# Performance work log

Hardware: AMD Instinct MI355X
Metric: run time of the kernel (lower is better)

## Reference

```python
import jax, jax.numpy as jnp
import numpy as np

B, T, C, SIZE = 2, 4096, 1024, 1024
ROPE_DIM = 64
GAMMA = 0.96


def setup_inputs() -> dict:
    key = jax.random.key(0)
    ks = jax.random.split(key, 8)
    x = jax.random.normal(ks[0], (B, T, C), dtype=jnp.float32)
    group_mask = jax.random.randint(ks[1], (B, T), 0, 2).astype(jnp.float32)
    att_mask = jnp.ones((B, T), dtype=jnp.float32)
    # torch init: randn(in, out) / in
    W_Q = jax.random.normal(ks[2], (C, SIZE), dtype=jnp.float32) / C
    W_K = jax.random.normal(ks[3], (C, SIZE), dtype=jnp.float32) / C
    W_V = jax.random.normal(ks[4], (C, SIZE), dtype=jnp.float32) / C
    fc_w = jax.random.normal(ks[5], (SIZE, SIZE), dtype=jnp.float32) / np.float32(np.sqrt(SIZE))
    fc_b = jnp.zeros((SIZE,), dtype=jnp.float32)
    return dict(x=x, group_mask=group_mask, att_mask=att_mask,
                W_Q=W_Q, W_K=W_K, W_V=W_V, fc_w=fc_w, fc_b=fc_b)


def _rope(t, offset):
    # lucidrains rotate_queries_or_keys: rotate first ROPE_DIM features of
    # the last dim, interleaved-pair rotation, positions along axis -2.
    seq = t.shape[-2]
    inv = 1.0 / (10000.0 ** (jnp.arange(0, ROPE_DIM, 2, dtype=jnp.float32) / ROPE_DIM))
    pos = jnp.arange(seq, dtype=jnp.float32) + offset
    freqs = pos[:, None] * inv[None, :]              # [T, D/2]
    freqs = jnp.repeat(freqs, 2, axis=-1)            # [T, D]
    cos, sin = jnp.cos(freqs), jnp.sin(freqs)
    t_rot, t_pass = t[..., :ROPE_DIM], t[..., ROPE_DIM:]
    x1, x2 = t_rot[..., 0::2], t_rot[..., 1::2]
    rot_half = jnp.stack([-x2, x1], axis=-1).reshape(t_rot.shape)
    t_rot = t_rot * cos + rot_half * sin
    return jnp.concatenate([t_rot, t_pass], axis=-1)


def reference(x, group_mask, att_mask, W_Q, W_K, W_V, fc_w, fc_b):
    Bx, Tx, _ = x.shape
    # _qkv with apply_rope=True, apply_act=True (ReLU)
    Q = jax.nn.relu(_rope(x @ W_Q, 0))               # [B,T,SIZE]
    K = jax.nn.relu(_rope(x @ W_K, 0))
    V = jax.nn.relu(x @ W_V)
    n = jnp.arange(Tx)[:, None]
    m = jnp.arange(Tx)[None, :]
    causal = (n >= m)
    # decay mask D[n,m] = gamma^(n-m) for n>=m else 0
    D = jnp.where(causal, jnp.float32(GAMMA) ** (n - m).astype(jnp.float32), 0.0)
    # group mask G[b,n,m] = group_mask[b, n-m] for n>=m else 0
    idx = jnp.clip(n - m, 0, Tx - 1)                 # [T,T]
    G = group_mask[:, idx] * causal.astype(x.dtype)  # [B,T,T]
    A = jnp.einsum('bnd,bmd->bnm', Q, K)
    A = A * att_mask[:, :, None]                     # attention mask
    A = A * D[None, :, :]                            # decay mask
    A = A * G                                        # group mask
    y = jnp.einsum('bnm,bmd->bnd', A, V)
    y = y @ fc_w + fc_b
    return y
```

## Files before the change

kernel.cpp:

```cpp
#include <hip/hip_runtime.h>
#include <stdint.h>

typedef __attribute__((ext_vector_type(4))) float f32x4;
typedef __attribute__((ext_vector_type(8))) __bf16 bf16x8;
typedef __attribute__((ext_vector_type(4))) unsigned short u16x4;
typedef __attribute__((ext_vector_type(8))) unsigned short u16x8;

#define DEV __device__ __forceinline__

DEV unsigned short f2bf(float f) {
  union { float f; unsigned int u; } v; v.f = f;
  unsigned int r = v.u + 0x7fffu + ((v.u >> 16) & 1u);
  return (unsigned short)(r >> 16);
}

DEV void gl_lds16(const void* g, void* l) {
  __builtin_amdgcn_global_load_lds(
      (const __attribute__((address_space(1))) unsigned int*)g,
      (__attribute__((address_space(3))) unsigned int*)l, 16, 0, 0);
}


__global__ void prep_rope(float* __restrict__ costab, float* __restrict__ sintab) {
  int idx = blockIdx.x * 256 + threadIdx.x;
  int n = idx >> 6, c = idx & 63, j = c >> 1;
  float inv = powf(10000.0f, -(float)(2 * j) / 64.0f);
  float ang = (float)n * inv;
  costab[idx] = cosf(ang);
  sintab[idx] = sinf(ang);
}

__global__ void prep_wtab(const float* __restrict__ gm, float* __restrict__ wtab) {
  int t = threadIdx.x;
  int b = t >> 9, d = t & 511;
  wtab[t] = gm[b * 4096 + d] * powf(0.96f, (float)d);
}

__global__ void cvt_x(const float* __restrict__ x, unsigned short* __restrict__ xb) {
  size_t i8 = ((size_t)blockIdx.x * 256 + threadIdx.x) * 8;
  float4 a = *(const float4*)(x + i8);
  float4 b = *(const float4*)(x + i8 + 4);
  u16x8 o;
  o[0] = f2bf(a.x); o[1] = f2bf(a.y); o[2] = f2bf(a.z); o[3] = f2bf(a.w);
  o[4] = f2bf(b.x); o[5] = f2bf(b.y); o[6] = f2bf(b.z); o[7] = f2bf(b.w);
  *(u16x8*)(xb + i8) = o;
}

__global__ void transpose_cvt(const float* __restrict__ src, unsigned short* __restrict__ dst) {
  __shared__ float tile[32][33];
  int tx = threadIdx.x & 31, ty = threadIdx.x >> 5;
  int c0 = blockIdx.x * 32, r0 = blockIdx.y * 32;
  #pragma unroll
  for (int j = 0; j < 4; j++)
    tile[ty + 8 * j][tx] = src[(size_t)(r0 + ty + 8 * j) * 1024 + c0 + tx];
  __syncthreads();
  #pragma unroll
  for (int j = 0; j < 4; j++)
    dst[(size_t)(c0 + ty + 8 * j) * 1024 + r0 + tx] = f2bf(tile[tx][ty + 8 * j]);
}

template<int EPI>
__global__ void __launch_bounds__(256, 2)
gemm128(const unsigned short* __restrict__ A,
        const unsigned short* __restrict__ Bt,
        unsigned short* __restrict__ q_out,
        unsigned short* __restrict__ k_out,
        unsigned short* __restrict__ vt_out,
        const float* __restrict__ costab,
        const float* __restrict__ sintab,
        float* __restrict__ f_out,
        const float* __restrict__ bias)
{
  constexpr int K = 1024;
  __shared__ char smem[32768];
  char* a_sm = smem;
  char* b_sm = smem + 16384;
  const int tid = threadIdx.x;
  const int lane = tid & 63;
  const int w = tid >> 6;
  const int wm = w >> 1, wn = w & 1;
  const int bm = blockIdx.x, bn = blockIdx.y;

  const f32x4 fz = {0.f, 0.f, 0.f, 0.f};
  f32x4 acc[4][4];
  #pragma unroll
  for (int i = 0; i < 4; i++)
    #pragma unroll
    for (int j = 0; j < 4; j++) acc[i][j] = fz;

  const unsigned short* Abase = A + (size_t)bm * 128 * K;
  const unsigned short* Bbase = Bt + (size_t)bn * 128 * K;

  for (int k0 = 0; k0 < K; k0 += 64) {
    __syncthreads();
    #pragma unroll
    for (int i = 0; i < 4; i++) {
      int tg = i * 256 + tid;
      int row = tg >> 3;
      int sl = (tg & 7) ^ (row & 7);
      gl_lds16(Abase + (size_t)row * K + k0 + sl * 8, a_sm + tg * 16);
    }
    #pragma unroll
    for (int i = 0; i < 4; i++) {
      int tg = i * 256 + tid;
      int row = tg >> 3;
      int sl = (tg & 7) ^ (row & 7);
      gl_lds16(Bbase + (size_t)row * K + k0 + sl * 8, b_sm + tg * 16);
    }
    __syncthreads();
    #pragma unroll
    for (int ks = 0; ks < 2; ks++) {
      int kb = ks * 64 + ((lane >> 4) << 4);
      bf16x8 af[4], bfv[4];
      #pragma unroll
      for (int f = 0; f < 4; f++) {
        int ar = wm * 64 + f * 16 + (lane & 15);
        af[f] = *(const bf16x8*)(a_sm + ar * 128 + (kb ^ ((ar & 7) << 4)));
        int br = wn * 64 + f * 16 + (lane & 15);
        bfv[f] = *(const bf16x8*)(b_sm + br * 128 + (kb ^ ((br & 7) << 4)));
      }
      #pragma unroll
      for (int fm = 0; fm < 4; fm++)
        #pragma unroll
        for (int fn = 0; fn < 4; fn++)
          acc[fm][fn] = __builtin_amdgcn_mfma_f32_16x16x32_bf16(af[fm], bfv[fn], acc[fm][fn], 0, 0, 0);
    }
  }

  const int rbase = bm * 128 + wm * 64 + ((lane >> 4) << 2);
  const int cbase = bn * 128 + wn * 64;

  if constexpr (EPI == 0) {
    #pragma unroll
    for (int fn = 0; fn < 4; fn++) {
      int col = cbase + fn * 16 + (lane & 15);
      int which = col >> 10;
      int c = col & 1023;
      #pragma unroll
      for (int fm = 0; fm < 4; fm++) {
        int row0 = rbase + fm * 16;
        float vals[4];
        #pragma unroll
        for (int r = 0; r < 4; r++) vals[r] = acc[fm][fn][r];
        if (which < 2) {
          if (c < 64) {
            #pragma unroll
            for (int r = 0; r < 4; r++) {
              float p = __shfl_xor(vals[r], 1);
              int n = (row0 + r) & 4095;
              float cs = costab[n * 64 + c];
              float sn = sintab[n * 64 + c];
              float rh = (c & 1) ? p : -p;
              vals[r] = vals[r] * cs + rh * sn;
            }
          }
          unsigned short* dst = (which == 0) ? q_out : k_out;
          #pragma unroll
          for (int r = 0; r < 4; r++) {
            float v = vals[r] > 0.f ? vals[r] : 0.f;
            dst[(size_t)(row0 + r) * 1024 + c] = f2bf(v);
          }
        } else {
          u16x4 sv;
          #pragma unroll
          for (int r = 0; r < 4; r++) {
            float v = vals[r] > 0.f ? vals[r] : 0.f;
            sv[r] = f2bf(v);
          }
          *(u16x4*)(vt_out + (size_t)c * 8192 + row0) = sv;
        }
      }
    }
  } else {
    #pragma unroll
    for (int fn = 0; fn < 4; fn++) {
      int col = cbase + fn * 16 + (lane & 15);
      float bv = bias[col];
      #pragma unroll
      for (int fm = 0; fm < 4; fm++) {
        int row0 = rbase + fm * 16;
        #pragma unroll
        for (int r = 0; r < 4; r++)
          f_out[(size_t)(row0 + r) * 1024 + col] = acc[fm][fn][r] + bv;
      }
    }
  }
}

__global__ void __launch_bounds__(512, 2)
attn_kernel(const unsigned short* __restrict__ Qb,
            const unsigned short* __restrict__ Kb,
            const unsigned short* __restrict__ Vt,
            const float* __restrict__ wtab,
            const float* __restrict__ att_mask,
            unsigned short* __restrict__ Yb)
{
  __shared__ char smem[49152];
  __shared__ float wl[320];
  char* k_sm = smem;
  char* q_sm = smem + 40960;
  char* p_sm = smem;

  const int tid = threadIdx.x;
  const int lane = tid & 63;
  const int w = tid >> 6;
  const int q0 = blockIdx.x * 64;
  const int b = blockIdx.y;
  const int base = b * 4096;
  const int kv0 = q0 - 256;

  if (tid < 320) wl[tid] = wtab[b * 512 + tid];

  const int wq = w >> 2, wk = w & 3;
  const f32x4 fz = {0.f, 0.f, 0.f, 0.f};
  f32x4 sacc[2][5];
  #pragma unroll
  for (int i = 0; i < 2; i++)
    #pragma unroll
    for (int j = 0; j < 5; j++) sacc[i][j] = fz;

  for (int c0 = 0; c0 < 1024; c0 += 64) {
    __syncthreads();
    {
      int row = tid >> 3;
      int sl = (tid & 7) ^ (row & 7);
      gl_lds16(Qb + (size_t)(base + q0 + row) * 1024 + c0 + sl * 8, q_sm + tid * 16);
    }
    #pragma unroll
    for (int i = 0; i < 5; i++) {
      int tg = i * 512 + tid;
      int row = tg >> 3;
      int sl = (tg & 7) ^ (row & 7);
      int m = kv0 + row; m = m < 0 ? 0 : m;
      gl_lds16(Kb + (size_t)(base + m) * 1024 + c0 + sl * 8, k_sm + tg * 16);
    }
    __syncthreads();
    #pragma unroll
    for (int ks = 0; ks < 2; ks++) {
      int kb = ks * 64 + ((lane >> 4) << 4);
      bf16x8 af[2], bfv[5];
      #pragma unroll
      for (int f = 0; f < 2; f++) {
        int ar = wq * 32 + f * 16 + (lane & 15);
        af[f] = *(const bf16x8*)(q_sm + ar * 128 + (kb ^ ((ar & 7) << 4)));
      }
      #pragma unroll
      for (int f = 0; f < 5; f++) {
        int br = wk * 80 + f * 16 + (lane & 15);
        bfv[f] = *(const bf16x8*)(k_sm + br * 128 + (kb ^ ((br & 7) << 4)));
      }
      #pragma unroll
      for (int fm = 0; fm < 2; fm++)
        #pragma unroll
        for (int fj = 0; fj < 5; fj++)
          sacc[fm][fj] = __builtin_amdgcn_mfma_f32_16x16x32_bf16(af[fm], bfv[fj], sacc[fm][fj], 0, 0, 0);
    }
  }
  __syncthreads();

  #pragma unroll
  for (int fm = 0; fm < 2; fm++) {
    #pragma unroll
    for (int fj = 0; fj < 5; fj++) {
      int jj = wk * 80 + fj * 16 + (lane & 15);
      int m = kv0 + jj;
      #pragma unroll
      for (int r = 0; r < 4; r++) {
        int i = wq * 32 + fm * 16 + ((lane >> 4) << 2) + r;
        int d = 256 + i - jj;
        float wgt = (d >= 0 && m >= 0) ? wl[d] : 0.f;
        *(unsigned short*)(p_sm + i * 640 + ((jj * 2) ^ ((i & 7) << 4))) =
            f2bf(sacc[fm][fj][r] * wgt);
      }
    }
  }
  __syncthreads();

  f32x4 yacc[4][8];
  #pragma unroll
  for (int i = 0; i < 4; i++)
    #pragma unroll
    for (int j = 0; j < 8; j++) yacc[i][j] = fz;

  for (int kt = 0; kt < 10; kt++) {
    int kb = kt * 64 + ((lane >> 4) << 4);
    bf16x8 pa[4], vb[8];
    #pragma unroll
    for (int f = 0; f < 4; f++) {
      int i = f * 16 + (lane & 15);
      pa[f] = *(const bf16x8*)(p_sm + i * 640 + (kb ^ ((i & 7) << 4)));
    }
    int kvi = kt * 32 + ((lane >> 4) << 3);
    int m = kv0 + kvi; m = m < 0 ? 0 : m;
    #pragma unroll
    for (int f = 0; f < 8; f++) {
      int col = w * 128 + f * 16 + (lane & 15);
      vb[f] = *(const bf16x8*)(Vt + (size_t)col * 8192 + base + m);
    }
    #pragma unroll
    for (int fm = 0; fm < 4; fm++)
      #pragma unroll
      for (int fn = 0; fn < 8; fn++)
        yacc[fm][fn] = __builtin_amdgcn_mfma_f32_16x16x32_bf16(pa[fm], vb[fn], yacc[fm][fn], 0, 0, 0);
  }

  #pragma unroll
  for (int fm = 0; fm < 4; fm++) {
    #pragma unroll
    for (int r = 0; r < 4; r++) {
      int n = q0 + fm * 16 + ((lane >> 4) << 2) + r;
      float am = att_mask[base + n];
      #pragma unroll
      for (int fn = 0; fn < 8; fn++) {
        int col = w * 128 + fn * 16 + (lane & 15);
        Yb[(size_t)(base + n) * 1024 + col] = f2bf(yacc[fm][fn][r] * am);
      }
    }
  }
}

extern "C" void kernel_launch(void* const* d_in, const int* in_sizes, int n_in,
                              void* d_out, int out_size, void* d_ws, size_t ws_size,
                              hipStream_t stream)
{
  (void)in_sizes; (void)n_in; (void)out_size;
  const float* x   = (const float*)d_in[0];
  const float* gm  = (const float*)d_in[1];
  const float* am  = (const float*)d_in[2];
  const float* wq  = (const float*)d_in[3];
  const float* wk  = (const float*)d_in[4];
  const float* wv  = (const float*)d_in[5];
  const float* fcw = (const float*)d_in[6];
  const float* fcb = (const float*)d_in[7];
  float* out = (float*)d_out;

  char* p = (char*)d_ws;
  unsigned short* xb    = (unsigned short*)p; p += (size_t)8192 * 1024 * 2;
  unsigned short* Qb    = (unsigned short*)p; p += (size_t)8192 * 1024 * 2;
  unsigned short* Kb    = (unsigned short*)p; p += (size_t)8192 * 1024 * 2;
  unsigned short* Vt    = (unsigned short*)p; p += (size_t)8192 * 1024 * 2;
  unsigned short* Ybuf  = (unsigned short*)p; p += (size_t)8192 * 1024 * 2;
  unsigned short* WqkvT = (unsigned short*)p; p += (size_t)3072 * 1024 * 2;
  unsigned short* FcwT  = (unsigned short*)p; p += (size_t)1024 * 1024 * 2;
  float* costab = (float*)p; p += (size_t)4096 * 64 * 4;
  float* sintab = (float*)p; p += (size_t)4096 * 64 * 4;
  float* wtab   = (float*)p; p += 4096;
  if ((size_t)(p - (char*)d_ws) > ws_size) return;

  prep_rope<<<1024, 256, 0, stream>>>(costab, sintab);
  prep_wtab<<<1, 1024, 0, stream>>>(gm, wtab);
  cvt_x<<<4096, 256, 0, stream>>>(x, xb);
  transpose_cvt<<<dim3(32, 32), 256, 0, stream>>>(wq, WqkvT);
  transpose_cvt<<<dim3(32, 32), 256, 0, stream>>>(wk, WqkvT + (size_t)1024 * 1024);
  transpose_cvt<<<dim3(32, 32), 256, 0, stream>>>(wv, WqkvT + (size_t)2048 * 1024);
  transpose_cvt<<<dim3(32, 32), 256, 0, stream>>>(fcw, FcwT);

  gemm128<0><<<dim3(64, 24), 256, 0, stream>>>(xb, WqkvT, Qb, Kb, Vt, costab, sintab, nullptr, nullptr);
  attn_kernel<<<dim3(64, 2), 512, 0, stream>>>(Qb, Kb, Vt, wtab, am, Ybuf);
  gemm128<1><<<dim3(64, 8), 256, 0, stream>>>(Ybuf, FcwT, nullptr, nullptr, nullptr, nullptr, nullptr, out, fcb);
}
```

Before: 244.9 us.

## Merge prep launches, remap GEMM blocks across XCDs, split attention into 32-row tiles

Fuses the rope and decay-table prep kernels into one launch and the four weight transposes into one 3D-grid launch, cutting launch overhead. Both GEMMs now use a 1D grid with an XCD-aware block remap (id&7 chunking) so neighbouring tiles share L2. The attention kernel moves from 64 to 32 query rows per block, doubling the grid to 256 blocks for better CU occupancy. It also drops the LDS staging of Q/K in favour of direct global bf16x8 loads, and adds a fast unclamped V-load path.

```diff
diff --git a/kernel.cpp b/kernel.cpp
--- a/kernel.cpp
+++ b/kernel.cpp
@@ -21,19 +21,19 @@
 }
 
 
-__global__ void prep_rope(float* __restrict__ costab, float* __restrict__ sintab) {
+__global__ void prep_tabs(const float* __restrict__ gm,
+                          float* __restrict__ costab, float* __restrict__ sintab,
+                          float* __restrict__ wtab) {
   int idx = blockIdx.x * 256 + threadIdx.x;
   int n = idx >> 6, c = idx & 63, j = c >> 1;
   float inv = powf(10000.0f, -(float)(2 * j) / 64.0f);
   float ang = (float)n * inv;
   costab[idx] = cosf(ang);
   sintab[idx] = sinf(ang);
-}
-
-__global__ void prep_wtab(const float* __restrict__ gm, float* __restrict__ wtab) {
-  int t = threadIdx.x;
-  int b = t >> 9, d = t & 511;
-  wtab[t] = gm[b * 4096 + d] * powf(0.96f, (float)d);
+  if (idx < 1024) {
+    int b = idx >> 9, d = idx & 511;
+    wtab[idx] = gm[b * 4096 + d] * powf(0.96f, (float)d);
+  }
 }
 
 __global__ void cvt_x(const float* __restrict__ x, unsigned short* __restrict__ xb) {
@@ -46,8 +46,13 @@
   *(u16x8*)(xb + i8) = o;
 }
 
-__global__ void transpose_cvt(const float* __restrict__ src, unsigned short* __restrict__ dst) {
+__global__ void transpose_cvt4(const float* __restrict__ s0, const float* __restrict__ s1,
+                               const float* __restrict__ s2, const float* __restrict__ s3,
+                               unsigned short* __restrict__ d0, unsigned short* __restrict__ d3) {
   __shared__ float tile[32][33];
+  int z = blockIdx.z;
+  const float* src = (z == 0) ? s0 : (z == 1) ? s1 : (z == 2) ? s2 : s3;
+  unsigned short* dst = (z == 3) ? d3 : d0 + (size_t)z * 1024 * 1024;
   int tx = threadIdx.x & 31, ty = threadIdx.x >> 5;
   int c0 = blockIdx.x * 32, r0 = blockIdx.y * 32;
   #pragma unroll
@@ -79,7 +84,12 @@
   const int lane = tid & 63;
   const int w = tid >> 6;
   const int wm = w >> 1, wn = w & 1;
-  const int bm = blockIdx.x, bn = blockIdx.y;
+
+  const int id = blockIdx.x;
+  const int chunk = gridDim.x >> 3;
+  const int nid = (id & 7) * chunk + (id >> 3);
+  const int bm = nid & 63;
+  const int bn = nid >> 6;
 
   const f32x4 fz = {0.f, 0.f, 0.f, 0.f};
   f32x4 acc[4][4];
@@ -195,124 +205,118 @@
             const float* __restrict__ att_mask,
             unsigned short* __restrict__ Yb)
 {
-  __shared__ char smem[49152];
-  __shared__ float wl[320];
-  char* k_sm = smem;
-  char* q_sm = smem + 40960;
-  char* p_sm = smem;
+  __shared__ alignas(16) unsigned char p_sm[32 * 640];
+  __shared__ float wl[512];
 
   const int tid = threadIdx.x;
   const int lane = tid & 63;
   const int w = tid >> 6;
-  const int q0 = blockIdx.x * 64;
-  const int b = blockIdx.y;
+
+  const int id = blockIdx.x + blockIdx.y * 128;
+  const int nid = (id & 7) * 32 + (id >> 3);
+  const int qb = nid & 127;
+  const int b = nid >> 7;
+
+  const int q0 = qb * 32;
   const int base = b * 4096;
   const int kv0 = q0 - 256;
 
-  if (tid < 320) wl[tid] = wtab[b * 512 + tid];
+  if (tid < 512) wl[tid] = wtab[b * 512 + tid];
 
   const int wq = w >> 2, wk = w & 3;
+  const int l15 = lane & 15, lhi = lane >> 4;
+
+  const unsigned short* qptr =
+      Qb + (size_t)(base + q0 + wq * 16 + l15) * 1024 + lhi * 8;
+  const unsigned short* krow[5];
+  #pragma unroll
+  for (int f = 0; f < 5; f++) {
+    int m = kv0 + wk * 80 + f * 16 + l15;
+    m = m < 0 ? 0 : (m > 4095 ? 4095 : m);
+    krow[f] = Kb + (size_t)(base + m) * 1024 + lhi * 8;
+  }
+
   const f32x4 fz = {0.f, 0.f, 0.f, 0.f};
-  f32x4 sacc[2][5];
+  f32x4 sacc[5];
+  #pragma unroll
+  for (int f = 0; f < 5; f++) sacc[f] = fz;
+
+  for (int kk = 0; kk < 32; ++kk) {
+    bf16x8 af = *(const bf16x8*)(qptr + kk * 32);
+    #pragma unroll
+    for (int f = 0; f < 5; f++) {
+      bf16x8 bfv = *(const bf16x8*)(krow[f] + kk * 32);
+      sacc[f] = __builtin_amdgcn_mfma_f32_16x16x32_bf16(af, bfv, sacc[f], 0, 0, 0);
+    }
+  }
+
+  __syncthreads();
+
+  #pragma unroll
+  for (int f = 0; f < 5; f++) {
+    int jj = wk * 80 + f * 16 + l15;
+    int m = kv0 + jj;
+    #pragma unroll
+    for (int r = 0; r < 4; r++) {
+      int i = wq * 16 + lhi * 4 + r;
+      int d = 256 + i - jj;
+      float wgt = (d >= 0 && m >= 0) ? wl[d] : 0.f;
+      *(unsigned short*)(p_sm + i * 640 + ((jj * 2) ^ ((i & 7) << 4))) =
+          f2bf(sacc[f][r] * wgt);
+    }
+  }
+  __syncthreads();
+
+  f32x4 yacc[2][8];
   #pragma unroll
   for (int i = 0; i < 2; i++)
     #pragma unroll
-    for (int j = 0; j < 5; j++) sacc[i][j] = fz;
-
-  for (int c0 = 0; c0 < 1024; c0 += 64) {
-    __syncthreads();
-    {
-      int row = tid >> 3;
-      int sl = (tid & 7) ^ (row & 7);
-      gl_lds16(Qb + (size_t)(base + q0 + row) * 1024 + c0 + sl * 8, q_sm + tid * 16);
-    }
-    #pragma unroll
-    for (int i = 0; i < 5; i++) {
-      int tg = i * 512 + tid;
-      int row = tg >> 3;
-      int sl = (tg & 7) ^ (row & 7);
-      int m = kv0 + row; m = m < 0 ? 0 : m;
-      gl_lds16(Kb + (size_t)(base + m) * 1024 + c0 + sl * 8, k_sm + tg * 16);
-    }
-    __syncthreads();
-    #pragma unroll
-    for (int ks = 0; ks < 2; ks++) {
-      int kb = ks * 64 + ((lane >> 4) << 4);
-      bf16x8 af[2], bfv[5];
-      #pragma unroll
-      for (int f = 0; f < 2; f++) {
-        int ar = wq * 32 + f * 16 + (lane & 15);
-        af[f] = *(const bf16x8*)(q_sm + ar * 128 + (kb ^ ((ar & 7) << 4)));
-      }
-      #pragma unroll
-      for (int f = 0; f < 5; f++) {
-        int br = wk * 80 + f * 16 + (lane & 15);
-        bfv[f] = *(const bf16x8*)(k_sm + br * 128 + (kb ^ ((br & 7) << 4)));
-      }
-      #pragma unroll
-      for (int fm = 0; fm < 2; fm++)
-        #pragma unroll
-        for (int fj = 0; fj < 5; fj++)
-          sacc[fm][fj] = __builtin_amdgcn_mfma_f32_16x16x32_bf16(af[fm], bfv[fj], sacc[fm][fj], 0, 0, 0);
-    }
-  }
-  __syncthreads();
-
-  #pragma unroll
-  for (int fm = 0; fm < 2; fm++) {
-    #pragma unroll
-    for (int fj = 0; fj < 5; fj++) {
-      int jj = wk * 80 + fj * 16 + (lane & 15);
-      int m = kv0 + jj;
-      #pragma unroll
-      for (int r = 0; r < 4; r++) {
-        int i = wq * 32 + fm * 16 + ((lane >> 4) << 2) + r;
-        int d = 256 + i - jj;
-        float wgt = (d >= 0 && m >= 0) ? wl[d] : 0.f;
-        *(unsigned short*)(p_sm + i * 640 + ((jj * 2) ^ ((i & 7) << 4))) =
-            f2bf(sacc[fm][fj][r] * wgt);
-      }
-    }
-  }
-  __syncthreads();
-
-  f32x4 yacc[4][8];
-  #pragma unroll
-  for (int i = 0; i < 4; i++)
-    #pragma unroll
     for (int j = 0; j < 8; j++) yacc[i][j] = fz;
 
-  for (int kt = 0; kt < 10; kt++) {
-    int kb = kt * 64 + ((lane >> 4) << 4);
-    bf16x8 pa[4], vb[8];
-    #pragma unroll
-    for (int f = 0; f < 4; f++) {
-      int i = f * 16 + (lane & 15);
-      pa[f] = *(const bf16x8*)(p_sm + i * 640 + (kb ^ ((i & 7) << 4)));
-    }
-    int kvi = kt * 32 + ((lane >> 4) << 3);
-    int m = kv0 + kvi; m = m < 0 ? 0 : m;
-    #pragma unroll
-    for (int f = 0; f < 8; f++) {
-      int col = w * 128 + f * 16 + (lane & 15);
-      vb[f] = *(const bf16x8*)(Vt + (size_t)col * 8192 + base + m);
-    }
-    #pragma unroll
-    for (int fm = 0; fm < 4; fm++)
+  const bool fastv = (kv0 >= 0) && (kv0 <= 3776);
+  const unsigned short* vptr[8];
+  #pragma unroll
+  for (int f = 0; f < 8; f++) {
+    int col = w * 128 + f * 16 + l15;
+    vptr[f] = Vt + (size_t)col * 8192 + base + kv0 + lhi * 8;
+  }
+
+  for (int kt = 0; kt < 10; ++kt) {
+    bf16x8 pa[2], vb[8];
+    #pragma unroll
+    for (int fm = 0; fm < 2; fm++) {
+      int row = fm * 16 + l15;
+      int cp = kt * 64 + lhi * 16;
+      pa[fm] = *(const bf16x8*)(p_sm + row * 640 + (cp ^ ((row & 7) << 4)));
+    }
+    if (fastv) {
+      #pragma unroll
+      for (int f = 0; f < 8; f++) vb[f] = *(const bf16x8*)(vptr[f] + kt * 32);
+    } else {
+      int m = kv0 + kt * 32 + lhi * 8;
+      m = m < 0 ? 0 : (m > 4088 ? 4088 : m);
+      #pragma unroll
+      for (int f = 0; f < 8; f++) {
+        int col = w * 128 + f * 16 + l15;
+        vb[f] = *(const bf16x8*)(Vt + (size_t)col * 8192 + base + m);
+      }
+    }
+    #pragma unroll
+    for (int fm = 0; fm < 2; fm++)
       #pragma unroll
       for (int fn = 0; fn < 8; fn++)
         yacc[fm][fn] = __builtin_amdgcn_mfma_f32_16x16x32_bf16(pa[fm], vb[fn], yacc[fm][fn], 0, 0, 0);
   }
 
   #pragma unroll
-  for (int fm = 0; fm < 4; fm++) {
+  for (int fm = 0; fm < 2; fm++) {
     #pragma unroll
     for (int r = 0; r < 4; r++) {
-      int n = q0 + fm * 16 + ((lane >> 4) << 2) + r;
+      int n = q0 + fm * 16 + lhi * 4 + r;
       float am = att_mask[base + n];
       #pragma unroll
       for (int fn = 0; fn < 8; fn++) {
-        int col = w * 128 + fn * 16 + (lane & 15);
+        int col = w * 128 + fn * 16 + l15;
         Yb[(size_t)(base + n) * 1024 + col] = f2bf(yacc[fm][fn][r] * am);
       }
     }
@@ -347,15 +351,11 @@
   float* wtab   = (float*)p; p += 4096;
   if ((size_t)(p - (char*)d_ws) > ws_size) return;
 
-  prep_rope<<<1024, 256, 0, stream>>>(costab, sintab);
-  prep_wtab<<<1, 1024, 0, stream>>>(gm, wtab);
+  prep_tabs<<<1024, 256, 0, stream>>>(gm, costab, sintab, wtab);
   cvt_x<<<4096, 256, 0, stream>>>(x, xb);
-  transpose_cvt<<<dim3(32, 32), 256, 0, stream>>>(wq, WqkvT);
-  transpose_cvt<<<dim3(32, 32), 256, 0, stream>>>(wk, WqkvT + (size_t)1024 * 1024);
-  transpose_cvt<<<dim3(32, 32), 256, 0, stream>>>(wv, WqkvT + (size_t)2048 * 1024);
-  transpose_cvt<<<dim3(32, 32), 256, 0, stream>>>(fcw, FcwT);
-
-  gemm128<0><<<dim3(64, 24), 256, 0, stream>>>(xb, WqkvT, Qb, Kb, Vt, costab, sintab, nullptr, nullptr);
-  attn_kernel<<<dim3(64, 2), 512, 0, stream>>>(Qb, Kb, Vt, wtab, am, Ybuf);
-  gemm128<1><<<dim3(64, 8), 256, 0, stream>>>(Ybuf, FcwT, nullptr, nullptr, nullptr, nullptr, nullptr, out, fcb);
-}
+  transpose_cvt4<<<dim3(32, 32, 4), 256, 0, stream>>>(wq, wk, wv, fcw, WqkvT, FcwT);
+
+  gemm128<0><<<1536, 256, 0, stream>>>(xb, WqkvT, Qb, Kb, Vt, costab, sintab, nullptr, nullptr);
+  attn_kernel<<<dim3(128, 2), 512, 0, stream>>>(Qb, Kb, Vt, wtab, am, Ybuf);
+  gemm128<1><<<512, 256, 0, stream>>>(Ybuf, FcwT, nullptr, nullptr, nullptr, nullptr, nullptr, out, fcb);
+}
```

Measured after the change: 276.3 us. 1.13x slower.
